# Kernel tuning notes

Measured on AMD Instinct MI355X. Metric: run time of the kernel, lower is better.

The kernel has to match this reference:

```python
import jax, jax.numpy as jnp
import numpy as np

N = 40000; E = 500000; IN = 128; ED = 16; HID = 64; HEADS = 4; OUT = 256; B = 128
NEG = 0.2  # GATv2 leaky_relu negative slope


def _add_self_loops(edge_index, edge_attr, n):
    # PyG add_self_loops with fill_value='mean': loop attr = mean of incoming edge attrs per node
    dst = edge_index[1]
    s = jax.ops.segment_sum(edge_attr, dst, num_segments=n)
    c = jax.ops.segment_sum(jnp.ones((edge_attr.shape[0],), edge_attr.dtype), dst, num_segments=n)
    loop_attr = s / jnp.maximum(c, 1.0)[:, None]
    loops = jnp.arange(n, dtype=edge_index.dtype)
    ei = jnp.concatenate([edge_index, jnp.stack([loops, loops])], axis=1)
    ea = jnp.concatenate([edge_attr, loop_attr], axis=0)
    return ei, ea


def _seg_softmax(logits, seg, n):
    m = jax.ops.segment_max(logits, seg, num_segments=n)
    m = jnp.where(jnp.isfinite(m), m, 0.0)  # guard empty segments
    e = jnp.exp(logits - m[seg])
    z = jax.ops.segment_sum(e, seg, num_segments=n)
    return e / (z[seg] + 1e-16)


def _gatv2(x, src, dst, ea, Wl, bl, Wr, br, We, att, bias, heads, oc, concat):
    n = x.shape[0]
    xl = (x @ Wl + bl).reshape(n, heads, oc)  # lin_l (source/message transform)
    xr = (x @ Wr + br).reshape(n, heads, oc)  # lin_r (target transform)
    ef = (ea @ We).reshape(-1, heads, oc)     # lin_edge (no bias)
    s = jax.nn.leaky_relu(xl[src] + xr[dst] + ef, NEG)  # [Etot,H,C]
    alpha = _seg_softmax(jnp.einsum('ehc,hc->eh', s, att), dst, n)  # scatter-softmax over dst
    out = jax.ops.segment_sum(xl[src] * alpha[..., None], dst, num_segments=n)  # [N,H,C]
    out = out.reshape(n, heads * oc) if concat else out.mean(axis=1)
    return out + bias


def setup_inputs():
    ks = jax.random.split(jax.random.key(0), 32)
    W = lambda i, shp: jax.random.normal(ks[i], shp, jnp.float32) * 0.05
    z = lambda d: jnp.zeros((d,), jnp.float32)
    H = HEADS * HID
    return dict(
        x=jax.random.normal(ks[0], (N, IN), jnp.float32),
        edge_index=jax.random.randint(ks[1], (2, E), 0, N),
        edge_attr=jax.random.normal(ks[2], (E, ED), jnp.float32),
        batch=jnp.sort(jax.random.randint(ks[3], (N,), 0, B)),
        batch_size=B,
        c1_Wl=W(4, (IN, H)), c1_bl=z(H), c1_Wr=W(5, (IN, H)), c1_br=z(H), c1_We=W(6, (ED, H)), c1_att=W(7, (HEADS, HID)), c1_bias=z(H),
        c2_Wl=W(8, (H, H)), c2_bl=z(H), c2_Wr=W(9, (H, H)), c2_br=z(H), c2_We=W(10, (ED, H)), c2_att=W(11, (HEADS, HID)), c2_bias=z(H),
        c3_Wl=W(12, (H, OUT)), c3_bl=z(OUT), c3_Wr=W(13, (H, OUT)), c3_br=z(OUT), c3_We=W(14, (ED, OUT)), c3_att=W(15, (1, OUT)), c3_bias=z(OUT),
        gate_W1=W(16, (OUT, 128)), gate_b1=z(128), gate_W2=W(17, (128, 1)), gate_b2=z(1),
        reg_W1=W(18, (OUT, 128)), reg_b1=z(128), reg_W2=W(19, (128, 2)), reg_b2=z(2),
    )


def reference(x, edge_index, edge_attr, batch, batch_size,
              c1_Wl, c1_bl, c1_Wr, c1_br, c1_We, c1_att, c1_bias,
              c2_Wl, c2_bl, c2_Wr, c2_br, c2_We, c2_att, c2_bias,
              c3_Wl, c3_bl, c3_Wr, c3_br, c3_We, c3_att, c3_bias,
              gate_W1, gate_b1, gate_W2, gate_b2,
              reg_W1, reg_b1, reg_W2, reg_b2):
    # task_type='homo_lumo' path; dropout disabled (inference)
    ei, ea = _add_self_loops(edge_index, edge_attr, N)
    src, dst = ei[0], ei[1]
    h = jax.nn.relu(_gatv2(x, src, dst, ea, c1_Wl, c1_bl, c1_Wr, c1_br, c1_We, c1_att, c1_bias, HEADS, HID, True))
    h = jax.nn.relu(_gatv2(h, src, dst, ea, c2_Wl, c2_bl, c2_Wr, c2_br, c2_We, c2_att, c2_bias, HEADS, HID, True))
    h = _gatv2(h, src, dst, ea, c3_Wl, c3_bl, c3_Wr, c3_br, c3_We, c3_att, c3_bias, 1, OUT, True)
    # AttentionalAggregation pooling
    gate = jax.nn.relu(h @ gate_W1 + gate_b1) @ gate_W2 + gate_b2  # [N,1]
    a = _seg_softmax(gate[:, 0], batch, batch_size)
    g = jax.ops.segment_sum(h * a[:, None], batch, num_segments=batch_size)  # [B,OUT]
    return jax.nn.relu(g @ reg_W1 + reg_b1) @ reg_W2 + reg_b2  # [B,2]
```

## Files before the change

### kernel.cpp

```cpp
#include <hip/hip_runtime.h>
#include <math.h>

constexpr int N_NODES = 40000;
constexpr int N_EDGES = 500000;
constexpr int ETOT    = N_EDGES + N_NODES;
constexpr int IN_DIM  = 128;
constexpr int ED_DIM  = 16;
constexpr int FEAT    = 256;
constexpr int BATCH   = 128;
constexpr float NEG   = 0.2f;
constexpr int NCHUNK  = (N_NODES + 255) / 256;

typedef float vfloat16 __attribute__((ext_vector_type(16)));

__global__ __launch_bounds__(256) void k_deg(const int* __restrict__ dst, int* __restrict__ deg)
{
    int e = blockIdx.x * 256 + threadIdx.x;
    if (e >= ETOT) return;
    int v = e < N_EDGES ? dst[e] : e - N_EDGES;
    atomicAdd(&deg[v], 1);
}

__global__ __launch_bounds__(256) void k_scan1(const int* __restrict__ deg, int* __restrict__ bsum)
{
    __shared__ int s[256];
    int t = threadIdx.x;
    int idx = blockIdx.x * 256 + t;
    s[t] = idx < N_NODES ? deg[idx] : 0;
    __syncthreads();
    for (int st = 128; st; st >>= 1) { if (t < st) s[t] += s[t + st]; __syncthreads(); }
    if (t == 0) bsum[blockIdx.x] = s[0];
}

__global__ __launch_bounds__(256) void k_scan2(const int* __restrict__ bsum,
    int* __restrict__ boff, int* __restrict__ rowptr)
{
    __shared__ int s[256];
    int t = threadIdx.x;
    int v = t < NCHUNK ? bsum[t] : 0;
    s[t] = v;
    __syncthreads();
    for (int off = 1; off < 256; off <<= 1) {
        int x = (t >= off) ? s[t - off] : 0;
        __syncthreads();
        s[t] += x;
        __syncthreads();
    }
    if (t < NCHUNK) boff[t] = s[t] - v;
    if (t == 0) rowptr[N_NODES] = ETOT;
}

__global__ __launch_bounds__(256) void k_scan3(const int* __restrict__ deg,
    const int* __restrict__ boff, int* __restrict__ rowptr)
{
    __shared__ int s[256];
    int t = threadIdx.x;
    int idx = blockIdx.x * 256 + t;
    int v = idx < N_NODES ? deg[idx] : 0;
    s[t] = v;
    __syncthreads();
    for (int off = 1; off < 256; off <<= 1) {
        int x = (t >= off) ? s[t - off] : 0;
        __syncthreads();
        s[t] += x;
        __syncthreads();
    }
    if (idx < N_NODES) rowptr[idx] = boff[blockIdx.x] + s[t] - v;
}

__global__ __launch_bounds__(256) void k_fill(const int* __restrict__ srcA, const int* __restrict__ dst,
    const int* __restrict__ rowptr, int* __restrict__ fill, int2* __restrict__ elist2)
{
    int e = blockIdx.x * 256 + threadIdx.x;
    if (e >= ETOT) return;
    int v = e < N_EDGES ? dst[e]  : e - N_EDGES;
    int s = e < N_EDGES ? srcA[e] : e - N_EDGES;
    int pos = rowptr[v] + atomicAdd(&fill[v], 1);
    elist2[pos] = make_int2(s, e);
}

__global__ __launch_bounds__(256) void k_loop_csr(const int2* __restrict__ elist2,
    const int* __restrict__ rowptr, const float* __restrict__ ea, float* __restrict__ loop_attr)
{
    int t = blockIdx.x * 256 + threadIdx.x;
    if (t >= N_NODES * ED_DIM) return;
    int n = t >> 4, d = t & 15;
    int p0 = rowptr[n], p1 = rowptr[n + 1];
    float s = 0.f; int c = 0;
    for (int p = p0; p < p1; ++p) {
        int e = elist2[p].y;
        if (e < N_EDGES) { s += ea[(size_t)e * ED_DIM + d]; ++c; }
    }
    loop_attr[t] = s / (float)(c > 0 ? c : 1);
}

__global__ __launch_bounds__(256) void k_gemm(const float* __restrict__ A, const float* __restrict__ W,
    const float* __restrict__ bias, float* __restrict__ C, int M, int N, int K, int act)
{
    __shared__ float As[16][136];
    __shared__ float Bs[16][136];
    int t = threadIdx.x;
    int bm = blockIdx.x * 128, bn = blockIdx.y * 128;
    int tr = t >> 4, tc = t & 15;
    int mr0 = tr * 8, nc0 = tc * 4;

    int ar0 = t >> 1,        ak0 = (t & 1) << 3;
    int bk0 = t >> 5,        bn0 = (t & 31) << 2;

    float acc[8][8] = {};

    int r0 = bm + ar0; r0 = r0 < M ? r0 : M - 1;
    float4 avA = *(const float4*)(A + (size_t)r0 * K + ak0);
    float4 avB = *(const float4*)(A + (size_t)r0 * K + ak0 + 4);
    float4 bvA = *(const float4*)(W + (size_t)bk0 * N + bn + bn0);
    float4 bvB = *(const float4*)(W + (size_t)(bk0 + 8) * N + bn + bn0);

    for (int k0 = 0; k0 < K; k0 += 16) {
        __syncthreads();
        As[ak0 + 0][ar0] = avA.x; As[ak0 + 1][ar0] = avA.y;
        As[ak0 + 2][ar0] = avA.z; As[ak0 + 3][ar0] = avA.w;
        As[ak0 + 4][ar0] = avB.x; As[ak0 + 5][ar0] = avB.y;
        As[ak0 + 6][ar0] = avB.z; As[ak0 + 7][ar0] = avB.w;
        *(float4*)&Bs[bk0][bn0]     = bvA;
        *(float4*)&Bs[bk0 + 8][bn0] = bvB;
        __syncthreads();
        if (k0 + 16 < K) {
            avA = *(const float4*)(A + (size_t)r0 * K + k0 + 16 + ak0);
            avB = *(const float4*)(A + (size_t)r0 * K + k0 + 16 + ak0 + 4);
            bvA = *(const float4*)(W + (size_t)(k0 + 16 + bk0) * N + bn + bn0);
            bvB = *(const float4*)(W + (size_t)(k0 + 24 + bk0) * N + bn + bn0);
        }
        #pragma unroll
        for (int k = 0; k < 16; ++k) {
            float4 a0 = *(const float4*)&As[k][mr0];
            float4 a1 = *(const float4*)&As[k][mr0 + 4];
            float4 b0 = *(const float4*)&Bs[k][nc0];
            float4 b1 = *(const float4*)&Bs[k][64 + nc0];
            float am[8] = {a0.x, a0.y, a0.z, a0.w, a1.x, a1.y, a1.z, a1.w};
            float bv[8] = {b0.x, b0.y, b0.z, b0.w, b1.x, b1.y, b1.z, b1.w};
            #pragma unroll
            for (int i = 0; i < 8; ++i)
                #pragma unroll
                for (int j = 0; j < 8; ++j)
                    acc[i][j] = fmaf(am[i], bv[j], acc[i][j]);
        }
    }

    float bb[8];
    #pragma unroll
    for (int j = 0; j < 4; ++j) { bb[j] = bias[bn + nc0 + j]; bb[j + 4] = bias[bn + 64 + nc0 + j]; }
    #pragma unroll
    for (int i = 0; i < 8; ++i) {
        int row = bm + mr0 + i;
        if (row >= M) break;
        float4 o0, o1;
        o0.x = acc[i][0] + bb[0]; o0.y = acc[i][1] + bb[1];
        o0.z = acc[i][2] + bb[2]; o0.w = acc[i][3] + bb[3];
        o1.x = acc[i][4] + bb[4]; o1.y = acc[i][5] + bb[5];
        o1.z = acc[i][6] + bb[6]; o1.w = acc[i][7] + bb[7];
        if (act) {
            o0.x = fmaxf(o0.x, 0.f); o0.y = fmaxf(o0.y, 0.f); o0.z = fmaxf(o0.z, 0.f); o0.w = fmaxf(o0.w, 0.f);
            o1.x = fmaxf(o1.x, 0.f); o1.y = fmaxf(o1.y, 0.f); o1.z = fmaxf(o1.z, 0.f); o1.w = fmaxf(o1.w, 0.f);
        }
        *(float4*)(C + (size_t)row * N + bn + nc0)      = o0;
        *(float4*)(C + (size_t)row * N + bn + 64 + nc0) = o1;
    }
}

static void launch_gemm(const float* A, const float* W, const float* bias, float* C,
                        int M, int N, int K, int act, hipStream_t stream)
{
    dim3 grid((M + 127) / 128, N / 128);
    k_gemm<<<grid, 256, 0, stream>>>(A, W, bias, C, M, N, K, act);
}


#define XELOAD(s) do {                                                                \
    int src_ = eS[s].x, e_ = eS[s].y;                                                 \
    const float4* eb4_ = reinterpret_cast<const float4*>(                             \
        (e_ < N_EDGES) ? ea + (size_t)e_ * ED_DIM                                     \
                       : loop_attr + (size_t)src_ * ED_DIM);                          \
    evS[s][0] = eb4_[0]; evS[s][1] = eb4_[1];                                         \
    evS[s][2] = eb4_[2]; evS[s][3] = eb4_[3];                                         \
    const float* xp_ = xl + (size_t)src_ * FEAT + base;                               \
    xlvS[s][0] = xp_[0];  xlvS[s][1] = xp_[16];                                       \
    xlvS[s][2] = xp_[32]; xlvS[s][3] = xp_[48];                                       \
} while (0)

#define COMPUTE(s) do {                                                               \
    float ef0_ = 0.f, ef1_ = 0.f, ef2_ = 0.f, ef3_ = 0.f;                             \
    const float* ed_ = (const float*)evS[s];                                          \
    _Pragma("unroll")                                                                 \
    for (int d_ = 0; d_ < ED_DIM; ++d_) {                                             \
        float a_ = ed_[d_];                                                           \
        ef0_ = fmaf(a_, weV0[d_], ef0_); ef1_ = fmaf(a_, weV1[d_], ef1_);             \
        ef2_ = fmaf(a_, weV2[d_], ef2_); ef3_ = fmaf(a_, weV3[d_], ef3_);             \
    }                                                                                 \
    float s0_ = xlvS[s][0] + xrv[0] + ef0_;                                           \
    float s1_ = xlvS[s][1] + xrv[1] + ef1_;                                           \
    float s2_ = xlvS[s][2] + xrv[2] + ef2_;                                           \
    float s3_ = xlvS[s][3] + xrv[3] + ef3_;                                           \
    s0_ = fmaxf(s0_, 0.f) + NEG * fminf(s0_, 0.f);                                    \
    s1_ = fmaxf(s1_, 0.f) + NEG * fminf(s1_, 0.f);                                    \
    s2_ = fmaxf(s2_, 0.f) + NEG * fminf(s2_, 0.f);                                    \
    s3_ = fmaxf(s3_, 0.f) + NEG * fminf(s3_, 0.f);                                    \
    float l_ = fmaf(s0_, attR[0], fmaf(s1_, attR[1], fmaf(s2_, attR[2], s3_ * attR[3])));\
    l_ += __shfl_xor(l_, 1, 64);                                                      \
    l_ += __shfl_xor(l_, 2, 64);                                                      \
    l_ += __shfl_xor(l_, 4, 64);                                                      \
    l_ += __shfl_xor(l_, 8, 64);                                                      \
    if (H == 1) { l_ += __shfl_xor(l_, 16, 64); l_ += __shfl_xor(l_, 32, 64); }       \
    float nm_ = fmaxf(m, l_);                                                         \
    float sc_ = __expf(m - nm_);                                                      \
    float w_  = __expf(l_ - nm_);                                                     \
    z = fmaf(z, sc_, w_);                                                             \
    m = nm_;                                                                          \
    acc[0] = fmaf(acc[0], sc_, w_ * xlvS[s][0]);                                      \
    acc[1] = fmaf(acc[1], sc_, w_ * xlvS[s][1]);                                      \
    acc[2] = fmaf(acc[2], sc_, w_ * xlvS[s][2]);                                      \
    acc[3] = fmaf(acc[3], sc_, w_ * xlvS[s][3]);                                      \
} while (0)

#define PIN_WE() asm volatile("" : "+v"(weV0), "+v"(weV1), "+v"(weV2), "+v"(weV3))

template <int H, int RELU>
__global__ __launch_bounds__(256, 3) void k_gat(
    const float* __restrict__ xl, const float* __restrict__ xr,
    const float* __restrict__ ea, const float* __restrict__ loop_attr,
    const int2* __restrict__ elist2, const int* __restrict__ rowptr,
    const float* __restrict__ We, const float* __restrict__ att,
    const float* __restrict__ bias, float* __restrict__ out)
{
    int t = threadIdx.x;
    int lane = t & 63;
    int n = __builtin_amdgcn_readfirstlane(blockIdx.x * 4 + (t >> 6));
    int q = lane >> 4;
    int u = lane & 15;
    int base = q * 64 + u;

    vfloat16 weV0, weV1, weV2, weV3;
    #pragma unroll
    for (int d = 0; d < ED_DIM; ++d) {
        weV0[d] = We[d * FEAT + base];
        weV1[d] = We[d * FEAT + base + 16];
        weV2[d] = We[d * FEAT + base + 32];
        weV3[d] = We[d * FEAT + base + 48];
    }
    PIN_WE();

    float attR[4], xrv[4];
    #pragma unroll
    for (int j = 0; j < 4; ++j) {
        attR[j] = att[base + 16 * j];
        xrv[j]  = xr[(size_t)n * FEAT + base + 16 * j];
    }

    float m = -INFINITY, z = 0.f;
    float acc[4] = {0.f, 0.f, 0.f, 0.f};

    int p0 = rowptr[n], p1 = rowptr[n + 1];
    int pe = p1 - 1;

    int2   eS[2];
    float4 evS[2][4];
    float  xlvS[2][4];

    eS[0] = elist2[p0];
    { int pc = p0 + 1 > pe ? pe : p0 + 1; eS[1] = elist2[pc]; }
    XELOAD(0);

    int p = p0;
    while (true) {
        PIN_WE();
        XELOAD(1);
        { int pn = p + 2 > pe ? pe : p + 2; eS[0] = elist2[pn]; }
        COMPUTE(0);
        if (++p >= p1) break;
        XELOAD(0);
        { int pn = p + 2 > pe ? pe : p + 2; eS[1] = elist2[pn]; }
        COMPUTE(1);
        if (++p >= p1) break;
    }

    float inv = 1.0f / (z + 1e-16f);
    #pragma unroll
    for (int j = 0; j < 4; ++j) {
        float o = fmaf(acc[j], inv, bias[base + 16 * j]);
        if (RELU) o = fmaxf(o, 0.f);
        out[(size_t)n * FEAT + base + 16 * j] = o;
    }
}

__global__ __launch_bounds__(256) void k_gate_score(const float* __restrict__ ghid,
    const float* __restrict__ W2, const float* __restrict__ b2, float* __restrict__ gate)
{
    int lane = threadIdx.x & 63;
    int n = blockIdx.x * 4 + (threadIdx.x >> 6);
    float v = ghid[(size_t)n * 128 + lane] * W2[lane] + ghid[(size_t)n * 128 + lane + 64] * W2[lane + 64];
    #pragma unroll
    for (int off = 32; off > 0; off >>= 1) v += __shfl_xor(v, off, 64);
    if (lane == 0) gate[n] = v + b2[0];
}

__device__ __forceinline__ int lbound(const int* a, int n, int v)
{
    int lo = 0, hi = n;
    while (lo < hi) { int mid = (lo + hi) >> 1; if (a[mid] < v) lo = mid + 1; else hi = mid; }
    return lo;
}

__global__ __launch_bounds__(256) void k_pool(const float* __restrict__ gate,
    const float* __restrict__ h, const int* __restrict__ batch, float* __restrict__ g)
{
    int b = blockIdx.x;
    int t = threadIdx.x;
    __shared__ float red[256];
    int start = lbound(batch, N_NODES, b);
    int end   = lbound(batch, N_NODES, b + 1);

    float mx = -INFINITY;
    for (int n = start + t; n < end; n += 256) mx = fmaxf(mx, gate[n]);
    red[t] = mx; __syncthreads();
    for (int s = 128; s; s >>= 1) { if (t < s) red[t] = fmaxf(red[t], red[t + s]); __syncthreads(); }
    float m = red[0];
    __syncthreads();

    float zs = 0.f;
    for (int n = start + t; n < end; n += 256) zs += __expf(gate[n] - m);
    red[t] = zs; __syncthreads();
    for (int s = 128; s; s >>= 1) { if (t < s) red[t] += red[t + s]; __syncthreads(); }
    float z = red[0];

    float gs = 0.f;
    for (int n = start; n < end; ++n) gs += __expf(gate[n] - m) * h[(size_t)n * FEAT + t];
    g[b * FEAT + t] = gs / (z + 1e-16f);
}

__global__ __launch_bounds__(128) void k_reg(const float* __restrict__ g,
    const float* __restrict__ W1, const float* __restrict__ b1,
    const float* __restrict__ W2, const float* __restrict__ b2, float* __restrict__ out)
{
    int b = blockIdx.x, t = threadIdx.x;
    __shared__ float sg[FEAT];
    sg[t] = g[b * FEAT + t];
    sg[t + 128] = g[b * FEAT + t + 128];
    __syncthreads();
    float hv = b1[t];
    for (int k = 0; k < FEAT; ++k) hv += sg[k] * W1[k * 128 + t];
    hv = fmaxf(hv, 0.f);
    __shared__ float p0s[128], p1s[128];
    p0s[t] = hv * W2[t * 2 + 0];
    p1s[t] = hv * W2[t * 2 + 1];
    __syncthreads();
    for (int s = 64; s; s >>= 1) {
        if (t < s) { p0s[t] += p0s[t + s]; p1s[t] += p1s[t + s]; }
        __syncthreads();
    }
    if (t == 0) { out[b * 2 + 0] = p0s[0] + b2[0]; out[b * 2 + 1] = p1s[0] + b2[1]; }
}

extern "C" void kernel_launch(void* const* d_in, const int* in_sizes, int n_in,
                              void* d_out, int out_size, void* d_ws, size_t ws_size,
                              hipStream_t stream)
{
    const float* x       = (const float*)d_in[0];
    const int*   ei      = (const int*)d_in[1];
    const float* ea      = (const float*)d_in[2];
    const int*   batch   = (const int*)d_in[3];
    const float* c1_Wl   = (const float*)d_in[5];
    const float* c1_bl   = (const float*)d_in[6];
    const float* c1_Wr   = (const float*)d_in[7];
    const float* c1_br   = (const float*)d_in[8];
    const float* c1_We   = (const float*)d_in[9];
    const float* c1_att  = (const float*)d_in[10];
    const float* c1_bias = (const float*)d_in[11];
    const float* c2_Wl   = (const float*)d_in[12];
    const float* c2_bl   = (const float*)d_in[13];
    const float* c2_Wr   = (const float*)d_in[14];
    const float* c2_br   = (const float*)d_in[15];
    const float* c2_We   = (const float*)d_in[16];
    const float* c2_att  = (const float*)d_in[17];
    const float* c2_bias = (const float*)d_in[18];
    const float* c3_Wl   = (const float*)d_in[19];
    const float* c3_bl   = (const float*)d_in[20];
    const float* c3_Wr   = (const float*)d_in[21];
    const float* c3_br   = (const float*)d_in[22];
    const float* c3_We   = (const float*)d_in[23];
    const float* c3_att  = (const float*)d_in[24];
    const float* c3_bias = (const float*)d_in[25];
    const float* gate_W1 = (const float*)d_in[26];
    const float* gate_b1 = (const float*)d_in[27];
    const float* gate_W2 = (const float*)d_in[28];
    const float* gate_b2 = (const float*)d_in[29];
    const float* reg_W1  = (const float*)d_in[30];
    const float* reg_b1  = (const float*)d_in[31];
    const float* reg_W2  = (const float*)d_in[32];
    const float* reg_b2  = (const float*)d_in[33];

    const int* srcArr = ei;
    const int* dstArr = ei + N_EDGES;

    float* ws = (float*)d_ws;
    size_t off = 0;
    auto alloc = [&](size_t nf) { float* p = ws + off; off += (nf + 63) & ~(size_t)63; return p; };
    float* xl        = alloc((size_t)N_NODES * FEAT);
    float* xr        = alloc((size_t)N_NODES * FEAT);
    float* h         = alloc((size_t)N_NODES * FEAT);
    float* loop_attr = alloc((size_t)N_NODES * ED_DIM);
    float* gpool     = alloc((size_t)BATCH * FEAT);
    int* ibase  = (int*)(ws + off);
    int* deg    = ibase;
    int* fill   = ibase + N_NODES;
    int* rowptr = ibase + 2 * N_NODES;
    int* bsum   = ibase + 3 * N_NODES + 64;
    int* boff   = bsum + 256;
    int2* elist2 = (int2*)(boff + 256);

    float* ghid = xl;
    float* gate = xr;

    hipMemsetAsync(deg, 0, (size_t)2 * N_NODES * sizeof(int), stream);

    k_deg<<<(ETOT + 255) / 256, 256, 0, stream>>>(dstArr, deg);
    k_scan1<<<NCHUNK, 256, 0, stream>>>(deg, bsum);
    k_scan2<<<1, 256, 0, stream>>>(bsum, boff, rowptr);
    k_scan3<<<NCHUNK, 256, 0, stream>>>(deg, boff, rowptr);
    k_fill<<<(ETOT + 255) / 256, 256, 0, stream>>>(srcArr, dstArr, rowptr, fill, elist2);
    k_loop_csr<<<(N_NODES * ED_DIM + 255) / 256, 256, 0, stream>>>(elist2, rowptr, ea, loop_attr);

    launch_gemm(x, c1_Wl, c1_bl, xl, N_NODES, FEAT, IN_DIM, 0, stream);
    launch_gemm(x, c1_Wr, c1_br, xr, N_NODES, FEAT, IN_DIM, 0, stream);
    k_gat<4, 1><<<N_NODES / 4, 256, 0, stream>>>(xl, xr, ea, loop_attr, elist2, rowptr,
                                                 c1_We, c1_att, c1_bias, h);
    launch_gemm(h, c2_Wl, c2_bl, xl, N_NODES, FEAT, FEAT, 0, stream);
    launch_gemm(h, c2_Wr, c2_br, xr, N_NODES, FEAT, FEAT, 0, stream);
    k_gat<4, 1><<<N_NODES / 4, 256, 0, stream>>>(xl, xr, ea, loop_attr, elist2, rowptr,
                                                 c2_We, c2_att, c2_bias, h);
    launch_gemm(h, c3_Wl, c3_bl, xl, N_NODES, FEAT, FEAT, 0, stream);
    launch_gemm(h, c3_Wr, c3_br, xr, N_NODES, FEAT, FEAT, 0, stream);
    k_gat<1, 0><<<N_NODES / 4, 256, 0, stream>>>(xl, xr, ea, loop_attr, elist2, rowptr,
                                                 c3_We, c3_att, c3_bias, h);

    launch_gemm(h, gate_W1, gate_b1, ghid, N_NODES, 128, FEAT, 1, stream);
    k_gate_score<<<N_NODES / 4, 256, 0, stream>>>(ghid, gate_W2, gate_b2, gate);
    k_pool<<<BATCH, 256, 0, stream>>>(gate, h, batch, gpool);
    k_reg<<<BATCH, 128, 0, stream>>>(gpool, reg_W1, reg_b1, reg_W2, reg_b2, (float*)d_out);
}
```

Before: 1.223 ms.

## Split GATv2 into edge-parallel logit kernel and node-wise online-softmax aggregation

Splits the fused per-destination GAT kernel in two. A new edge-parallel kernel computes the attention logits, one wave per head over 128-edge chunks, and writes them to a buffer. A lighter aggregation kernel then reads those logits and runs the online softmax and weighted sum. The edge list widens to int4 so it also carries the destination. This takes the 16-wide edge-feature projection and its register pressure out of the gather loop and balances work across high-degree nodes. In exchange it adds an extra logit buffer round-trip through memory, larger edge-list records and one more launch per layer.

```diff
diff --git a/kernel.cpp b/kernel.cpp
--- a/kernel.cpp
+++ b/kernel.cpp
@@ -10,8 +10,7 @@
 constexpr int BATCH   = 128;
 constexpr float NEG   = 0.2f;
 constexpr int NCHUNK  = (N_NODES + 255) / 256;
-
-typedef float vfloat16 __attribute__((ext_vector_type(16)));
+constexpr int LCH     = 128;
 
 __global__ __launch_bounds__(256) void k_deg(const int* __restrict__ dst, int* __restrict__ deg)
 {
@@ -69,17 +68,17 @@
 }
 
 __global__ __launch_bounds__(256) void k_fill(const int* __restrict__ srcA, const int* __restrict__ dst,
-    const int* __restrict__ rowptr, int* __restrict__ fill, int2* __restrict__ elist2)
+    const int* __restrict__ rowptr, int* __restrict__ fill, int4* __restrict__ elist4)
 {
     int e = blockIdx.x * 256 + threadIdx.x;
     if (e >= ETOT) return;
     int v = e < N_EDGES ? dst[e]  : e - N_EDGES;
     int s = e < N_EDGES ? srcA[e] : e - N_EDGES;
     int pos = rowptr[v] + atomicAdd(&fill[v], 1);
-    elist2[pos] = make_int2(s, e);
-}
-
-__global__ __launch_bounds__(256) void k_loop_csr(const int2* __restrict__ elist2,
+    elist4[pos] = make_int4(s, e, v, 0);
+}
+
+__global__ __launch_bounds__(256) void k_loop_csr(const int4* __restrict__ elist4,
     const int* __restrict__ rowptr, const float* __restrict__ ea, float* __restrict__ loop_attr)
 {
     int t = blockIdx.x * 256 + threadIdx.x;
@@ -88,7 +87,7 @@
     int p0 = rowptr[n], p1 = rowptr[n + 1];
     float s = 0.f; int c = 0;
     for (int p = p0; p < p1; ++p) {
-        int e = elist2[p].y;
+        int e = elist4[p].y;
         if (e < N_EDGES) { s += ea[(size_t)e * ED_DIM + d]; ++c; }
     }
     loop_attr[t] = s / (float)(c > 0 ? c : 1);
@@ -174,42 +173,64 @@
     k_gemm<<<grid, 256, 0, stream>>>(A, W, bias, C, M, N, K, act);
 }
 
-
-#define XELOAD(s) do {                                                                \
-    int src_ = eS[s].x, e_ = eS[s].y;                                                 \
-    const float4* eb4_ = reinterpret_cast<const float4*>(                             \
-        (e_ < N_EDGES) ? ea + (size_t)e_ * ED_DIM                                     \
-                       : loop_attr + (size_t)src_ * ED_DIM);                          \
-    evS[s][0] = eb4_[0]; evS[s][1] = eb4_[1];                                         \
-    evS[s][2] = eb4_[2]; evS[s][3] = eb4_[3];                                         \
-    const float* xp_ = xl + (size_t)src_ * FEAT + base;                               \
+__global__ __launch_bounds__(256) void k_logit(
+    const float* __restrict__ xl, const float* __restrict__ xr,
+    const float* __restrict__ ea, const float* __restrict__ loop_attr,
+    const int4* __restrict__ elist4, const float* __restrict__ We,
+    const float* __restrict__ att, float* __restrict__ lg)
+{
+    int t = threadIdx.x;
+    int w = t >> 6;
+
+    float weF[ED_DIM];
+    #pragma unroll
+    for (int d = 0; d < ED_DIM; ++d) weF[d] = We[d * FEAT + t];
+    float attT = att[t];
+
+    int p0 = blockIdx.x * LCH;
+    int p1 = p0 + LCH; p1 = p1 < ETOT ? p1 : ETOT;
+
+    for (int pos = p0; pos < p1; ++pos) {
+        int4 e4 = elist4[pos];
+        const float* eaP = (e4.y < N_EDGES) ? ea + (size_t)e4.y * ED_DIM
+                                            : loop_attr + (size_t)e4.x * ED_DIM;
+        float4 q0 = ((const float4*)eaP)[0];
+        float4 q1 = ((const float4*)eaP)[1];
+        float4 q2 = ((const float4*)eaP)[2];
+        float4 q3 = ((const float4*)eaP)[3];
+        float ev[ED_DIM] = {q0.x,q0.y,q0.z,q0.w, q1.x,q1.y,q1.z,q1.w,
+                            q2.x,q2.y,q2.z,q2.w, q3.x,q3.y,q3.z,q3.w};
+
+        float u = xl[(size_t)e4.x * FEAT + t] + xr[(size_t)e4.z * FEAT + t];
+        #pragma unroll
+        for (int d = 0; d < ED_DIM; ++d) u = fmaf(ev[d], weF[d], u);
+        u = fmaxf(u, 0.f) + NEG * fminf(u, 0.f);
+        float v = u * attT;
+
+        v += __shfl_xor(v, 1, 64);
+        v += __shfl_xor(v, 2, 64);
+        v += __shfl_xor(v, 4, 64);
+        v += __shfl_xor(v, 8, 64);
+        v += __shfl_xor(v, 16, 64);
+        v += __shfl_xor(v, 32, 64);
+
+        if ((t & 63) == 0) lg[pos * 4 + w] = v;
+    }
+}
+
+#define AGG_LOAD(s, pp) do {                                                          \
+    int pos_ = (pp);                                                                  \
+    srcS[s] = elist4[pos_].x;                                                         \
+    float4 lv_ = ((const float4*)lg)[pos_];                                           \
+    lS[s] = (H == 4) ? (q == 0 ? lv_.x : q == 1 ? lv_.y : q == 2 ? lv_.z : lv_.w)     \
+                     : (lv_.x + lv_.y + lv_.z + lv_.w);                               \
+    const float* xp_ = xl + (size_t)srcS[s] * FEAT + base;                            \
     xlvS[s][0] = xp_[0];  xlvS[s][1] = xp_[16];                                       \
     xlvS[s][2] = xp_[32]; xlvS[s][3] = xp_[48];                                       \
 } while (0)
 
-#define COMPUTE(s) do {                                                               \
-    float ef0_ = 0.f, ef1_ = 0.f, ef2_ = 0.f, ef3_ = 0.f;                             \
-    const float* ed_ = (const float*)evS[s];                                          \
-    _Pragma("unroll")                                                                 \
-    for (int d_ = 0; d_ < ED_DIM; ++d_) {                                             \
-        float a_ = ed_[d_];                                                           \
-        ef0_ = fmaf(a_, weV0[d_], ef0_); ef1_ = fmaf(a_, weV1[d_], ef1_);             \
-        ef2_ = fmaf(a_, weV2[d_], ef2_); ef3_ = fmaf(a_, weV3[d_], ef3_);             \
-    }                                                                                 \
-    float s0_ = xlvS[s][0] + xrv[0] + ef0_;                                           \
-    float s1_ = xlvS[s][1] + xrv[1] + ef1_;                                           \
-    float s2_ = xlvS[s][2] + xrv[2] + ef2_;                                           \
-    float s3_ = xlvS[s][3] + xrv[3] + ef3_;                                           \
-    s0_ = fmaxf(s0_, 0.f) + NEG * fminf(s0_, 0.f);                                    \
-    s1_ = fmaxf(s1_, 0.f) + NEG * fminf(s1_, 0.f);                                    \
-    s2_ = fmaxf(s2_, 0.f) + NEG * fminf(s2_, 0.f);                                    \
-    s3_ = fmaxf(s3_, 0.f) + NEG * fminf(s3_, 0.f);                                    \
-    float l_ = fmaf(s0_, attR[0], fmaf(s1_, attR[1], fmaf(s2_, attR[2], s3_ * attR[3])));\
-    l_ += __shfl_xor(l_, 1, 64);                                                      \
-    l_ += __shfl_xor(l_, 2, 64);                                                      \
-    l_ += __shfl_xor(l_, 4, 64);                                                      \
-    l_ += __shfl_xor(l_, 8, 64);                                                      \
-    if (H == 1) { l_ += __shfl_xor(l_, 16, 64); l_ += __shfl_xor(l_, 32, 64); }       \
+#define AGG_COMPUTE(s) do {                                                           \
+    float l_ = lS[s];                                                                 \
     float nm_ = fmaxf(m, l_);                                                         \
     float sc_ = __expf(m - nm_);                                                      \
     float w_  = __expf(l_ - nm_);                                                     \
@@ -221,14 +242,10 @@
     acc[3] = fmaf(acc[3], sc_, w_ * xlvS[s][3]);                                      \
 } while (0)
 
-#define PIN_WE() asm volatile("" : "+v"(weV0), "+v"(weV1), "+v"(weV2), "+v"(weV3))
-
 template <int H, int RELU>
-__global__ __launch_bounds__(256, 3) void k_gat(
-    const float* __restrict__ xl, const float* __restrict__ xr,
-    const float* __restrict__ ea, const float* __restrict__ loop_attr,
-    const int2* __restrict__ elist2, const int* __restrict__ rowptr,
-    const float* __restrict__ We, const float* __restrict__ att,
+__global__ __launch_bounds__(256) void k_agg(
+    const float* __restrict__ xl, const float* __restrict__ lg,
+    const int4* __restrict__ elist4, const int* __restrict__ rowptr,
     const float* __restrict__ bias, float* __restrict__ out)
 {
     int t = threadIdx.x;
@@ -238,47 +255,25 @@
     int u = lane & 15;
     int base = q * 64 + u;
 
-    vfloat16 weV0, weV1, weV2, weV3;
-    #pragma unroll
-    for (int d = 0; d < ED_DIM; ++d) {
-        weV0[d] = We[d * FEAT + base];
-        weV1[d] = We[d * FEAT + base + 16];
-        weV2[d] = We[d * FEAT + base + 32];
-        weV3[d] = We[d * FEAT + base + 48];
-    }
-    PIN_WE();
-
-    float attR[4], xrv[4];
-    #pragma unroll
-    for (int j = 0; j < 4; ++j) {
-        attR[j] = att[base + 16 * j];
-        xrv[j]  = xr[(size_t)n * FEAT + base + 16 * j];
-    }
-
     float m = -INFINITY, z = 0.f;
     float acc[4] = {0.f, 0.f, 0.f, 0.f};
 
     int p0 = rowptr[n], p1 = rowptr[n + 1];
     int pe = p1 - 1;
 
-    int2   eS[2];
-    float4 evS[2][4];
-    float  xlvS[2][4];
-
-    eS[0] = elist2[p0];
-    { int pc = p0 + 1 > pe ? pe : p0 + 1; eS[1] = elist2[pc]; }
-    XELOAD(0);
+    int   srcS[2];
+    float lS[2];
+    float xlvS[2][4];
+
+    AGG_LOAD(0, p0);
 
     int p = p0;
     while (true) {
-        PIN_WE();
-        XELOAD(1);
-        { int pn = p + 2 > pe ? pe : p + 2; eS[0] = elist2[pn]; }
-        COMPUTE(0);
+        { int pn = p + 1 > pe ? pe : p + 1; AGG_LOAD(1, pn); }
+        AGG_COMPUTE(0);
         if (++p >= p1) break;
-        XELOAD(0);
-        { int pn = p + 2 > pe ? pe : p + 2; eS[1] = elist2[pn]; }
-        COMPUTE(1);
+        { int pn = p + 1 > pe ? pe : p + 1; AGG_LOAD(0, pn); }
+        AGG_COMPUTE(1);
         if (++p >= p1) break;
     }
 
@@ -408,13 +403,14 @@
     float* h         = alloc((size_t)N_NODES * FEAT);
     float* loop_attr = alloc((size_t)N_NODES * ED_DIM);
     float* gpool     = alloc((size_t)BATCH * FEAT);
+    float* lg        = alloc((size_t)ETOT * 4);
     int* ibase  = (int*)(ws + off);
     int* deg    = ibase;
     int* fill   = ibase + N_NODES;
     int* rowptr = ibase + 2 * N_NODES;
     int* bsum   = ibase + 3 * N_NODES + 64;
     int* boff   = bsum + 256;
-    int2* elist2 = (int2*)(boff + 256);
+    int4* elist4 = (int4*)(boff + 256);
 
     float* ghid = xl;
     float* gate = xr;
@@ -425,21 +421,23 @@
     k_scan1<<<NCHUNK, 256, 0, stream>>>(deg, bsum);
     k_scan2<<<1, 256, 0, stream>>>(bsum, boff, rowptr);
     k_scan3<<<NCHUNK, 256, 0, stream>>>(deg, boff, rowptr);
-    k_fill<<<(ETOT + 255) / 256, 256, 0, stream>>>(srcArr, dstArr, rowptr, fill, elist2);
-    k_loop_csr<<<(N_NODES * ED_DIM + 255) / 256, 256, 0, stream>>>(elist2, rowptr, ea, loop_attr);
+    k_fill<<<(ETOT + 255) / 256, 256, 0, stream>>>(srcArr, dstArr, rowptr, fill, elist4);
+    k_loop_csr<<<(N_NODES * ED_DIM + 255) / 256, 256, 0, stream>>>(elist4, rowptr, ea, loop_attr);
+
+    int lblocks = (ETOT + LCH - 1) / LCH;
 
     launch_gemm(x, c1_Wl, c1_bl, xl, N_NODES, FEAT, IN_DIM, 0, stream);
     launch_gemm(x, c1_Wr, c1_br, xr, N_NODES, FEAT, IN_DIM, 0, stream);
-    k_gat<4, 1><<<N_NODES / 4, 256, 0, stream>>>(xl, xr, ea, loop_attr, elist2, rowptr,
-                                                 c1_We, c1_att, c1_bias, h);
+    k_logit<<<lblocks, 256, 0, stream>>>(xl, xr, ea, loop_attr, elist4, c1_We, c1_att, lg);
+    k_agg<4, 1><<<N_NODES / 4, 256, 0, stream>>>(xl, lg, elist4, rowptr, c1_bias, h);
     launch_gemm(h, c2_Wl, c2_bl, xl, N_NODES, FEAT, FEAT, 0, stream);
     launch_gemm(h, c2_Wr, c2_br, xr, N_NODES, FEAT, FEAT, 0, stream);
-    k_gat<4, 1><<<N_NODES / 4, 256, 0, stream>>>(xl, xr, ea, loop_attr, elist2, rowptr,
-                                                 c2_We, c2_att, c2_bias, h);
+    k_logit<<<lblocks, 256, 0, stream>>>(xl, xr, ea, loop_attr, elist4, c2_We, c2_att, lg);
+    k_agg<4, 1><<<N_NODES / 4, 256, 0, stream>>>(xl, lg, elist4, rowptr, c2_bias, h);
     launch_gemm(h, c3_Wl, c3_bl, xl, N_NODES, FEAT, FEAT, 0, stream);
     launch_gemm(h, c3_Wr, c3_br, xr, N_NODES, FEAT, FEAT, 0, stream);
-    k_gat<1, 0><<<N_NODES / 4, 256, 0, stream>>>(xl, xr, ea, loop_attr, elist2, rowptr,
-                                                 c3_We, c3_att, c3_bias, h);
+    k_logit<<<lblocks, 256, 0, stream>>>(xl, xr, ea, loop_attr, elist4, c3_We, c3_att, lg);
+    k_agg<1, 0><<<N_NODES / 4, 256, 0, stream>>>(xl, lg, elist4, rowptr, c3_bias, h);
 
     launch_gemm(h, gate_W1, gate_b1, ghid, N_NODES, 128, FEAT, 1, stream);
     k_gate_score<<<N_NODES / 4, 256, 0, stream>>>(ghid, gate_W2, gate_b2, gate);
```

Result: slower. 1.916 ms (+56.7%).
